# Kernel tuning notes

Measured on AMD Instinct MI355X. Metric: run time of the kernel, lower is better.

## Reference

```python
import jax, jax.numpy as jnp
import numpy as np

B, T, V, Dw, Df, H, L, F_ = 16, 96, 32000, 512, 512, 1024, 100, 64
EPS = 1e-8
SOS = 0


def setup_inputs() -> dict:
    key = jax.random.key(0)
    ks = jax.random.split(key, 24)
    rn = lambda k, s, sc=0.02: (jax.random.normal(k, s) * sc).astype(jnp.float32)
    pos_mask = (jax.random.uniform(ks[1], (B, F_, L)) < 0.3).astype(jnp.float32)
    pos_mask = jnp.maximum(pos_mask, jax.nn.one_hot(jnp.zeros((B, F_), jnp.int32), L))
    return {
        "fact_embeddings": rn(ks[0], (B, F_, Df), 1.0),
        "pos_mask": pos_mask,
        "emb": rn(ks[2], (V, Dw), 0.05),
        "W_ih": rn(ks[3], (4 * H, Df + Dw + L)),
        "W_hh": rn(ks[4], (4 * H, H)),
        "b_ih": jnp.zeros(4 * H, jnp.float32),
        "b_hh": jnp.zeros(4 * H, jnp.float32),
        "Wf1": rn(ks[5], (H, H + Df)), "bf1": jnp.zeros(H, jnp.float32),
        "Wf2": rn(ks[6], (Df, H)), "bf2": jnp.zeros(Df, jnp.float32),
        "Wc1": rn(ks[7], (H, H + Df)), "bc1": jnp.zeros(H, jnp.float32),
        "Wc2": rn(ks[8], (1, H)), "bc2": jnp.zeros(1, jnp.float32),
        "Wv1": rn(ks[9], (H, H + Df)), "bv1": jnp.zeros(H, jnp.float32),
        "Wv2": rn(ks[10], (Dw, H)), "bv2": jnp.zeros(Dw, jnp.float32),
        "Wp1": rn(ks[11], (H, H + Df)), "bp1": jnp.zeros(H, jnp.float32),
        "Wp2": rn(ks[12], (100, H)), "bp2": jnp.zeros(100, jnp.float32),
        "WP": rn(ks[13], (L, 100)), "bP": jnp.zeros(L, jnp.float32),
        "true_w": jax.random.randint(ks[14], (B, T), 0, L),
        "true_a": jax.random.randint(ks[15], (B, T), 0, F_),
        "true_z": jax.random.randint(ks[16], (B, T), 0, 2),
        "num_facts": jax.random.randint(ks[17], (B,), 1, F_),
    }


def reference(fact_embeddings, pos_mask, emb, W_ih, W_hh, b_ih, b_hh,
              Wf1, bf1, Wf2, bf2, Wc1, bc1, Wc2, bc2,
              Wv1, bv1, Wv2, bv2, Wp1, bp1, Wp2, bp2, WP, bP,
              true_w, true_a, true_z, num_facts):
    def mlp(x, W1, b1, W2, b2):
        return W2 @ jax.nn.relu(W1 @ x + b1) + b2

    def single(fe, pmask_b, tw, ta, tz, nf):
        # fe: [F_, Df]  pmask_b: [F_, L]  tw/ta/tz: [T]
        idx = jnp.arange(F_)
        valid = (idx < nf).astype(jnp.float32)
        attn_mask = jnp.where(idx == F_ - 1, 1.0, valid)  # NaF slot always allowed
        e_k = (fe * valid[:, None]).sum(0) / nf.astype(jnp.float32)

        def step(carry, inputs):
            a_prev, h, c, wv, wo = carry
            w_t, a_true, z_true = inputs
            x = jnp.concatenate([a_prev, wv, wo])  # [Df+Dw+L]
            gates = W_ih @ x + b_ih + W_hh @ h + b_hh
            i_g, f_g, g_g, o_g = jnp.split(gates, 4)
            c = jax.nn.sigmoid(f_g) * c + jax.nn.sigmoid(i_g) * jnp.tanh(g_g)
            h = jax.nn.sigmoid(o_g) * jnp.tanh(c)
            oe = jnp.concatenate([h, e_k])
            k_fact = mlp(oe, Wf1, bf1, Wf2, bf2)           # [Df]
            prob_a = jax.nn.softmax(fe @ k_fact)           # [F_]
            m = attn_mask * prob_a + EPS
            m = m / m.sum()
            log_m = jnp.log(m)
            a_idx = jnp.argmax(m)
            a_vec = fe[a_idx]
            oa = jnp.concatenate([h, a_vec])
            z = jax.nn.sigmoid(mlp(oa, Wc1, bc1, Wc2, bc2))[0]
            k_voca = mlp(oa, Wv1, bv1, Wv2, bv2)           # [Dw]
            log_w = jax.nn.log_softmax(emb @ k_voca)       # [V]
            k_pos = mlp(oa, Wp1, bp1, Wp2, bp2)            # [100]
            prob_pos = jax.nn.softmax(WP @ k_pos + bP)     # [L]
            mp = pmask_b[a_true] * prob_pos + EPS
            mp = mp / mp.sum()
            log_pos = jnp.log(mp)
            zf = z_true.astype(jnp.float32)
            loss = (-log_m[a_true]
                    + jnp.where(z_true == 0, -log_w[w_t], -log_pos[w_t])
                    - (zf * jnp.log(z) + (1.0 - zf) * jnp.log(1.0 - z)))
            wv_next = jnp.where(z_true == 0, emb[w_t], jnp.zeros(Dw, jnp.float32))
            wo_next = jnp.where(z_true == 0, jnp.zeros(L, jnp.float32), jax.nn.one_hot(w_t, L))
            return (a_vec, h, c, wv_next, wo_next), loss

        carry0 = (jnp.zeros(Df, jnp.float32), jnp.zeros(H, jnp.float32),
                  jnp.zeros(H, jnp.float32), emb[SOS], jnp.zeros(L, jnp.float32))
        _, losses = jax.lax.scan(step, carry0, (tw, ta, tz))
        return losses.sum()

    return jax.vmap(single)(fact_embeddings, pos_mask, true_w, true_a, true_z, num_facts).sum()
```

## Files before the change

### kernel.cpp

```cpp
#include <hip/hip_runtime.h>
#include <math.h>

#define TT 96
#define VV 32000
#define EPSF 1e-8f

typedef __attribute__((ext_vector_type(8))) short short8;
typedef __attribute__((ext_vector_type(4))) float f4v;

__device__ __forceinline__ float wsum64(float v){
  #pragma unroll
  for (int m=32;m>0;m>>=1) v += __shfl_xor(v,m);
  return v;
}
__device__ __forceinline__ float sigm(float x){ return 1.0f/(1.0f+expf(-x)); }
__device__ __forceinline__ float softplus(float x){ return x>20.0f ? x : log1pf(expf(x)); }
__device__ __forceinline__ float bf2f(unsigned short u){ return __uint_as_float(((unsigned)u)<<16); }
__device__ __forceinline__ unsigned short f2bf(float f){
  unsigned u = __float_as_uint(f);
  return (unsigned short)((u + 0x7fffu + ((u>>16)&1u)) >> 16);
}

__device__ __forceinline__ void st_dc(float* p, float v){
  __hip_atomic_store(p, v, __ATOMIC_RELAXED, __HIP_MEMORY_SCOPE_AGENT);
}
__device__ __forceinline__ void st_dc_i(int* p, int v){
  __hip_atomic_store(p, v, __ATOMIC_RELAXED, __HIP_MEMORY_SCOPE_AGENT);
}
__device__ __forceinline__ int ld_dc_i(const int* p){
  return __hip_atomic_load(p, __ATOMIC_RELAXED, __HIP_MEMORY_SCOPE_AGENT);
}
__device__ __forceinline__ float2 ld_dc_2(const float* p){
  union { unsigned long long u; float2 f; } cv;
  cv.u = __hip_atomic_load((const unsigned long long*)p, __ATOMIC_RELAXED, __HIP_MEMORY_SCOPE_AGENT);
  return cv.f;
}

__device__ __forceinline__ void gbar(unsigned* cnt, unsigned target){
  __syncthreads();
  if (threadIdx.x == 0){
    __hip_atomic_fetch_add(cnt, 1u, __ATOMIC_RELAXED, __HIP_MEMORY_SCOPE_AGENT);
    while (__hip_atomic_load(cnt, __ATOMIC_RELAXED, __HIP_MEMORY_SCOPE_AGENT) < target){
      __builtin_amdgcn_s_sleep(8);
    }
    asm volatile("" ::: "memory");
  }
  __syncthreads();
}

__device__ __forceinline__ void core_chunk(
  const float4* __restrict__ w0, const float4* __restrict__ w1,
  const float4* __restrict__ w2, const float4* __restrict__ w3,
  const float4* __restrict__ xl, int l, int g, float (&acc)[4][4])
{
  #pragma unroll
  for (int kt=0; kt<8; kt++){
    int i = kt*16 + l;
    float4 a0=w0[i], a1=w1[i], a2=w2[i], a3=w3[i];
    #pragma unroll
    for (int j=0;j<4;j++){
      float4 x = xl[(4*g+j)*129 + i];
      acc[0][j] += a0.x*x.x + a0.y*x.y + a0.z*x.z + a0.w*x.w;
      acc[1][j] += a1.x*x.x + a1.y*x.y + a1.z*x.z + a1.w*x.w;
      acc[2][j] += a2.x*x.x + a2.y*x.y + a2.z*x.z + a2.w*x.w;
      acc[3][j] += a3.x*x.x + a3.y*x.y + a3.z*x.z + a3.w*x.w;
    }
  }
}

__device__ __forceinline__ float reduce_pick(float (&acc)[4][4], int l){
  float r = 0.f;
  #pragma unroll
  for (int ri=0;ri<4;ri++)
  #pragma unroll
  for (int j=0;j<4;j++){
    float v = acc[ri][j];
    v += __shfl_xor(v,1); v += __shfl_xor(v,2);
    v += __shfl_xor(v,4); v += __shfl_xor(v,8);
    if (l == ri*4+j) r = v;
  }
  return r;
}

__global__ __launch_bounds__(256) void k_phase1(
  const float* __restrict__ Whh, float* __restrict__ hall,
  const float* __restrict__ Pw, const float* __restrict__ Pa,
  int* __restrict__ aall, float* __restrict__ c,
  const float* __restrict__ Wf1, const float* __restrict__ cf,
  float* __restrict__ tf,
  const float* __restrict__ Gb, const float* __restrict__ gb0,
  const int* __restrict__ ta, const int* __restrict__ nfp,
  float* __restrict__ loss, unsigned* __restrict__ bar)
{
  __shared__ float4 xl[16*129];
  __shared__ float sg[256];
  __shared__ float sS[64];
  int tid = threadIdx.x, lane = tid & 63, wave = tid >> 6;
  int l = lane & 15, g = lane >> 4;
  int wg = blockIdx.x;
  unsigned rnd = 0;

  for (int t=0; t<TT; t++){
    {
      int j0 = wg*4;
      const float4* h4 = (const float4*)hall + (size_t)t*4096;
      float acc[4][4] = {};
      for (int kc=0; kc<2; kc++){
        for (int idx=tid; idx<2048; idx+=256){
          int b = idx>>7, i = idx&127;
          xl[b*129+i] = h4[b*256 + kc*128 + i];
        }
        __syncthreads();
        const float4* w0 = (const float4*)(Whh + (size_t)(wave*1024 + j0+0)*1024) + kc*128;
        const float4* w1 = (const float4*)(Whh + (size_t)(wave*1024 + j0+1)*1024) + kc*128;
        const float4* w2 = (const float4*)(Whh + (size_t)(wave*1024 + j0+2)*1024) + kc*128;
        const float4* w3 = (const float4*)(Whh + (size_t)(wave*1024 + j0+3)*1024) + kc*128;
        core_chunk(w0,w1,w2,w3, xl, l, g, acc);
        __syncthreads();
      }
      float v = reduce_pick(acc, l);
      int r = l>>2;
      int b = g*4 + (l&3);
      int row = wave*1024 + j0 + r;
      float e = Pw[((size_t)(b*96+t))*4096 + row];
      if (t > 0){
        int ai = ld_dc_i(&aall[(t-1)*64 + b]);
        e += Pa[((size_t)(b*64+ai))*4096 + row];
      }
      sg[wave*64 + r*16 + b] = v + e;
      __syncthreads();
      if (tid < 64){
        int jj = j0 + (tid>>4), bb = tid&15;
        float ig = sg[  0 + (tid>>4)*16 + bb];
        float fg = sg[ 64 + (tid>>4)*16 + bb];
        float gg = sg[128 + (tid>>4)*16 + bb];
        float og = sg[192 + (tid>>4)*16 + bb];
        int ci = bb*1024 + jj;
        float cn = sigm(fg)*c[ci] + sigm(ig)*tanhf(gg);
        c[ci] = cn;
        st_dc(&hall[((size_t)(t+1)*16 + bb)*1024 + jj], sigm(og)*tanhf(cn));
      }
    }
    rnd++; gbar(bar, rnd*256u);

    if (wg < 64){
      int rl0 = wg*16 + wave*4;
      const float4* h4 = (const float4*)hall + (size_t)(t+1)*4096;
      float acc[4][4] = {};
      for (int kc=0; kc<2; kc++){
        for (int idx=tid; idx<2048; idx+=256){
          int b = idx>>7, i = idx&127;
          xl[b*129+i] = h4[b*256 + kc*128 + i];
        }
        __syncthreads();
        const float4* w0 = (const float4*)(Wf1 + (size_t)(rl0+0)*1536) + kc*128;
        const float4* w1 = (const float4*)(Wf1 + (size_t)(rl0+1)*1536) + kc*128;
        const float4* w2 = (const float4*)(Wf1 + (size_t)(rl0+2)*1536) + kc*128;
        const float4* w3 = (const float4*)(Wf1 + (size_t)(rl0+3)*1536) + kc*128;
        core_chunk(w0,w1,w2,w3, xl, l, g, acc);
        __syncthreads();
      }
      float v = reduce_pick(acc, l);
      int rl = rl0 + (l>>2);
      int b = g*4 + (l&3);
      st_dc(&tf[b*1024 + rl], fmaxf(v + cf[b*1024 + rl], 0.f));
    }
    rnd++; gbar(bar, rnd*256u);

    if (wg < 16){
      int b = wg;
      float* stf = (float*)xl;
      {
        const float* src = tf + b*1024;
        float2 c0 = ld_dc_2(src + 4*tid + 0);
        float2 c1 = ld_dc_2(src + 4*tid + 2);
        ((float2*)stf)[2*tid+0] = c0;
        ((float2*)stf)[2*tid+1] = c1;
      }
      __syncthreads();
      int f = tid>>2, q = tid&3;
      const float4* G4 = (const float4*)(Gb + (size_t)(b*64+f)*1024);
      const float4* st4 = (const float4*)stf;
      float acc = 0.f;
      for (int j=0;j<64;j++){
        int i = q*64 + j;
        float4 a = G4[i], x = st4[i];
        acc += a.x*x.x + a.y*x.y + a.z*x.z + a.w*x.w;
      }
      acc += __shfl_xor(acc,1);
      acc += __shfl_xor(acc,2);
      if (q==0) sS[f] = acc + gb0[b*64+f];
      __syncthreads();
      if (tid < 64){
        int nf = nfp[b];
        float s = sS[tid];
        float mx = s;
        #pragma unroll
        for (int m=32;m>0;m>>=1) mx = fmaxf(mx, __shfl_xor(mx,m));
        float p = expf(s - mx);
        float ps = wsum64(p);
        p /= ps;
        bool mask = (tid < nf) || (tid == 63);
        float mval = mask ? (p + EPSF) : EPSF;
        float msum = wsum64(mval);
        float bv = mval; int bi2 = tid;
        #pragma unroll
        for (int m=32;m>0;m>>=1){
          float ov = __shfl_xor(bv,m); int oi = __shfl_xor(bi2,m);
          if (ov > bv || (ov == bv && oi < bi2)){ bv = ov; bi2 = oi; }
        }
        int at = ta[b*TT + t];
        float mat = __shfl(mval, at);
        if (tid == 0){
          atomicAdd(loss, -(logf(mat) - logf(msum)));
          st_dc_i(&aall[t*64 + b], bi2);
        }
      }
      __syncthreads();
    }
    rnd++; gbar(bar, rnd*256u);
  }
}


__global__ __launch_bounds__(256) void k2_cvp(
  const float* __restrict__ Wc1, const float* __restrict__ Wv1,
  const float* __restrict__ Wp1, const float* __restrict__ hall,
  const float* __restrict__ Ph, const int* __restrict__ aall,
  const float* __restrict__ bc1, const float* __restrict__ bv1,
  const float* __restrict__ bp1, float* __restrict__ tcvp)
{
  __shared__ float4 xl[16*129];
  int tid = threadIdx.x, lane = tid & 63, wave = tid >> 6;
  int l = lane & 15, g = lane >> 4;
  int seg = blockIdx.x >> 6;
  int rl0 = (blockIdx.x & 63)*16 + wave*4;
  const float* W = (seg==0)?Wc1:(seg==1)?Wv1:Wp1;
  const float4* h4 = (const float4*)hall + (size_t)(16 + blockIdx.y*16)*256;
  float acc[4][4] = {};
  for (int kc=0; kc<2; kc++){
    for (int idx=tid; idx<2048; idx+=256){
      int cc = idx>>7, i = idx&127;
      xl[cc*129+i] = h4[cc*256 + kc*128 + i];
    }
    __syncthreads();
    const float4* w0 = (const float4*)(W + (size_t)(rl0+0)*1536) + kc*128;
    const float4* w1 = (const float4*)(W + (size_t)(rl0+1)*1536) + kc*128;
    const float4* w2 = (const float4*)(W + (size_t)(rl0+2)*1536) + kc*128;
    const float4* w3 = (const float4*)(W + (size_t)(rl0+3)*1536) + kc*128;
    core_chunk(w0,w1,w2,w3, xl, l, g, acc);
    __syncthreads();
  }
  float v = reduce_pick(acc, l);
  int rl = rl0 + (l>>2);
  int n = blockIdx.y*16 + g*4 + (l&3);
  int b = n & 15;
  int ai = aall[(n>>4)*64 + (n&15)];
  const float* bias = (seg==0)?bc1:(seg==1)?bv1:bp1;
  float vv = v + Ph[((size_t)(b*64+ai))*3072 + seg*1024 + rl] + bias[rl];
  tcvp[(size_t)n*3072 + seg*1024 + rl] = fmaxf(vv, 0.f);
}

__global__ __launch_bounds__(256) void k2_heads2(
  const float* __restrict__ Wv2, const float* __restrict__ bv2,
  const float* __restrict__ Wp2, const float* __restrict__ bp2,
  const float* __restrict__ Wc2, const float* __restrict__ bc2,
  const float* __restrict__ tcvp, unsigned short* __restrict__ kvh,
  float* __restrict__ kpall, float* __restrict__ zlall)
{
  __shared__ float4 xl[16*129];
  int tid = threadIdx.x, lane = tid & 63, wave = tid >> 6;
  int l = lane & 15, g = lane >> 4;
  int bx = blockIdx.x;
  int seg = (bx < 32) ? 0 : (bx < 39) ? 1 : 2;
  int rb  = (seg==0) ? bx*16 : (seg==1) ? (bx-32)*16 : 0;
  int rl0 = rb + wave*4;
  const float* WS = (seg==0)?Wv2:(seg==1)?Wp2:Wc2;
  int maxr = (seg==0)?511:(seg==1)?99:0;
  int xoff4 = (seg==0)?256:(seg==1)?512:0;
  const float4* X4 = (const float4*)tcvp;
  float acc[4][4] = {};
  for (int kc=0; kc<2; kc++){
    for (int idx=tid; idx<2048; idx+=256){
      int cc = idx>>7, i = idx&127;
      xl[cc*129+i] = X4[(size_t)(blockIdx.y*16+cc)*768 + xoff4 + kc*128 + i];
    }
    __syncthreads();
    const float4* w0 = (const float4*)(WS + (size_t)min(rl0+0,maxr)*1024) + kc*128;
    const float4* w1 = (const float4*)(WS + (size_t)min(rl0+1,maxr)*1024) + kc*128;
    const float4* w2 = (const float4*)(WS + (size_t)min(rl0+2,maxr)*1024) + kc*128;
    const float4* w3 = (const float4*)(WS + (size_t)min(rl0+3,maxr)*1024) + kc*128;
    core_chunk(w0,w1,w2,w3, xl, l, g, acc);
    __syncthreads();
  }
  float v = reduce_pick(acc, l);
  int rl = rl0 + (l>>2);
  int n = blockIdx.y*16 + g*4 + (l&3);
  if (seg==0) kvh[(size_t)n*512 + rl] = f2bf(v + bv2[rl]);
  else if (seg==1){ if (rl < 100) kpall[n*128 + rl] = v + bp2[rl]; }
  else { if (rl == 0) zlall[n] = v + bc2[0]; }
}

__global__ __launch_bounds__(256) void k2_vocab(
  const unsigned short* __restrict__ embh, const unsigned short* __restrict__ kvh,
  float2* __restrict__ part)
{
  int wid = blockIdx.x*4 + (threadIdx.x>>6);
  int lane = threadIdx.x & 63;
  int mtile = wid % 500, ntile = wid / 500;
  int mrow = mtile*64 + (lane&15);
  int ncol = ntile*64 + (lane&15);
  int ko = (lane>>4)*8;
  f4v acc[4][4];
  #pragma unroll
  for (int i=0;i<4;i++)
  #pragma unroll
  for (int j=0;j<4;j++)
  #pragma unroll
  for (int r=0;r<4;r++) acc[i][j][r] = 0.f;
  for (int kk=0; kk<512; kk+=32){
    short8 af[4], bfr[4];
    #pragma unroll
    for (int i=0;i<4;i++)
      af[i] = *(const short8*)(embh + (size_t)(mrow+16*i)*512 + kk + ko);
    #pragma unroll
    for (int i=0;i<4;i++)
      bfr[i] = *(const short8*)(kvh + (size_t)(ncol+16*i)*512 + kk + ko);
    #pragma unroll
    for (int i=0;i<4;i++)
      #pragma unroll
      for (int j=0;j<4;j++)
        acc[i][j] = __builtin_amdgcn_mfma_f32_16x16x32_bf16(af[i], bfr[j], acc[i][j], 0,0,0);
  }
  int q = lane>>4;
  #pragma unroll
  for (int j=0;j<4;j++){
    float mx = -3.4e38f;
    #pragma unroll
    for (int i=0;i<4;i++)
    #pragma unroll
    for (int r=0;r<4;r++) mx = fmaxf(mx, acc[i][j][r]);
    mx = fmaxf(mx, __shfl_xor(mx,16));
    mx = fmaxf(mx, __shfl_xor(mx,32));
    float s = 0.f;
    #pragma unroll
    for (int i=0;i<4;i++)
    #pragma unroll
    for (int r=0;r<4;r++) s += expf(acc[i][j][r] - mx);
    s += __shfl_xor(s,16);
    s += __shfl_xor(s,32);
    if (q==0){
      int col = ntile*64 + 16*j + (lane&15);
      part[(size_t)col*500 + mtile] = make_float2(mx, s);
    }
  }
}

__global__ __launch_bounds__(256) void k2_vfin(
  const float2* __restrict__ part, const unsigned short* __restrict__ embh,
  const unsigned short* __restrict__ kvh, const int* __restrict__ tw,
  const int* __restrict__ tz, float* __restrict__ loss)
{
  __shared__ float red[4];
  int n = blockIdx.x, tid = threadIdx.x;
  int t = n>>4, b = n&15;
  float mx = -3.4e38f;
  for (int i=tid; i<500; i+=256) mx = fmaxf(mx, part[(size_t)n*500+i].x);
  #pragma unroll
  for (int m=32;m>0;m>>=1) mx = fmaxf(mx, __shfl_xor(mx,m));
  if ((tid&63)==0) red[tid>>6] = mx;
  __syncthreads();
  float M = fmaxf(fmaxf(red[0],red[1]), fmaxf(red[2],red[3]));
  __syncthreads();
  float s = 0.f;
  for (int i=tid; i<500; i+=256){
    float2 p = part[(size_t)n*500+i];
    s += p.y * expf(p.x - M);
  }
  s = wsum64(s);
  if ((tid&63)==0) red[tid>>6] = s;
  __syncthreads();
  float S = red[0]+red[1]+red[2]+red[3];
  __syncthreads();
  int w = tw[b*96+t];
  float d = 0.f;
  {
    const unsigned short* er = embh + (size_t)w*512;
    const unsigned short* kr = kvh + (size_t)n*512;
    for (int i=tid; i<512; i+=256) d += bf2f(er[i])*bf2f(kr[i]);
  }
  d = wsum64(d);
  if ((tid&63)==0) red[tid>>6] = d;
  __syncthreads();
  if (tid==0 && tz[b*96+t]==0){
    float D = red[0]+red[1]+red[2]+red[3];
    atomicAdd(loss, -(D - (M + logf(S))));
  }
}

__global__ __launch_bounds__(128) void k2_posz(
  const float* __restrict__ kpall, const float* __restrict__ zlall,
  const float* __restrict__ WP, const float* __restrict__ bP,
  const float* __restrict__ pmask, const int* __restrict__ tw,
  const int* __restrict__ ta, const int* __restrict__ tz,
  float* __restrict__ loss)
{
  __shared__ float pp[100];
  int n = blockIdx.x, tid = threadIdx.x;
  int t = n>>4, b = n&15;
  if (tid < 100){
    float s = bP[tid];
    const float* wr = WP + tid*100;
    const float* kp = kpall + n*128;
    for (int j=0;j<100;j++) s += wr[j]*kp[j];
    pp[tid] = s;
  }
  __syncthreads();
  if (tid == 0){
    float u = zlall[n];
    int z = tz[b*96+t], w = tw[b*96+t], at = ta[b*96+t];
    float tot = z ? softplus(-u) : softplus(u);
    if (z){
      float mxv = -1e30f;
      for (int l2=0;l2<100;l2++) mxv = fmaxf(mxv, pp[l2]);
      float se = 0.f;
      for (int l2=0;l2<100;l2++) se += expf(pp[l2]-mxv);
      const float* pm = pmask + ((size_t)b*64 + at)*100;
      float msum = 0.f, mw = 0.f;
      for (int l2=0;l2<100;l2++){
        float m = pm[l2]*(expf(pp[l2]-mxv)/se) + EPSF;
        msum += m;
        if (l2==w) mw = m;
      }
      tot += -(logf(mw) - logf(msum));
    }
    atomicAdd(loss, tot);
  }
}


__global__ void k_cvt_emb(const float* __restrict__ emb, unsigned* __restrict__ out){
  const int n = VV*512/2;
  for (int idx = blockIdx.x*256 + threadIdx.x; idx < n; idx += gridDim.x*256){
    float2 v = ((const float2*)emb)[idx];
    unsigned a = __float_as_uint(v.x), b = __float_as_uint(v.y);
    unsigned ra = (a + 0x7fffu + ((a>>16)&1u)) >> 16;
    unsigned rb = (b + 0x7fffu + ((b>>16)&1u)) >> 16;
    out[idx] = ra | (rb<<16);
  }
}

__global__ void k_setup(const float* __restrict__ fe, const int* __restrict__ nfp,
                        float* __restrict__ e_k){
  int b = blockIdx.x, tid = threadIdx.x;
  int nf = nfp[b];
  for (int d=tid; d<512; d+=256){
    float s = 0.f;
    for (int f=0; f<nf; f++) s += fe[((size_t)b*64+f)*512 + d];
    e_k[b*512+d] = s/(float)nf;
  }
}

__global__ __launch_bounds__(256) void k_pre_pa(
  const float* __restrict__ Wih, const float* __restrict__ fe, float* __restrict__ Pa)
{
  __shared__ float4 xl[16*129];
  int tid = threadIdx.x, lane = tid & 63, wave = tid >> 6;
  int l = lane & 15, g = lane >> 4;
  int row0 = blockIdx.x*16 + wave*4;
  int c0 = blockIdx.y*16;
  const float4* fe4 = (const float4*)fe;
  for (int idx=tid; idx<2048; idx+=256){
    int cc = idx>>7, i = idx&127;
    xl[cc*129+i] = fe4[(size_t)(c0+cc)*128 + i];
  }
  __syncthreads();
  const float4* w0 = (const float4*)(Wih + (size_t)(row0+0)*1124);
  const float4* w1 = (const float4*)(Wih + (size_t)(row0+1)*1124);
  const float4* w2 = (const float4*)(Wih + (size_t)(row0+2)*1124);
  const float4* w3 = (const float4*)(Wih + (size_t)(row0+3)*1124);
  float acc[4][4] = {};
  core_chunk(w0,w1,w2,w3, xl, l, g, acc);
  float v = reduce_pick(acc, l);
  int row = row0 + (l>>2), c = c0 + g*4 + (l&3);
  Pa[(size_t)c*4096 + row] = v;
}

__global__ __launch_bounds__(256) void k_pre_ph(
  const float* __restrict__ Wc1, const float* __restrict__ Wv1,
  const float* __restrict__ Wp1, const float* __restrict__ fe, float* __restrict__ Ph)
{
  __shared__ float4 xl[16*129];
  int tid = threadIdx.x, lane = tid & 63, wave = tid >> 6;
  int l = lane & 15, g = lane >> 4;
  int row0 = blockIdx.x*16 + wave*4;
  int head = row0 >> 10, rl0 = row0 & 1023;
  const float* W = (head==0)?Wc1:(head==1)?Wv1:Wp1;
  int c0 = blockIdx.y*16;
  const float4* fe4 = (const float4*)fe;
  for (int idx=tid; idx<2048; idx+=256){
    int cc = idx>>7, i = idx&127;
    xl[cc*129+i] = fe4[(size_t)(c0+cc)*128 + i];
  }
  __syncthreads();
  const float4* w0 = (const float4*)(W + (size_t)(rl0+0)*1536 + 1024);
  const float4* w1 = (const float4*)(W + (size_t)(rl0+1)*1536 + 1024);
  const float4* w2 = (const float4*)(W + (size_t)(rl0+2)*1536 + 1024);
  const float4* w3 = (const float4*)(W + (size_t)(rl0+3)*1536 + 1024);
  float acc[4][4] = {};
  core_chunk(w0,w1,w2,w3, xl, l, g, acc);
  float v = reduce_pick(acc, l);
  int row = row0 + (l>>2), c = c0 + g*4 + (l&3);
  Ph[(size_t)c*3072 + row] = v;
}

__global__ __launch_bounds__(256) void k_pre_pw(
  const float* __restrict__ Wih, const float* __restrict__ emb,
  const int* __restrict__ tw, const int* __restrict__ tz,
  const float* __restrict__ bih, const float* __restrict__ bhh,
  float* __restrict__ Pw)
{
  __shared__ float4 xl[16*129];
  int tid = threadIdx.x, lane = tid & 63, wave = tid >> 6;
  int l = lane & 15, g = lane >> 4;
  int row0 = blockIdx.x*16 + wave*4;
  int c0 = blockIdx.y*16;
  for (int idx=tid; idx<2048; idx+=256){
    int cc = idx>>7, i = idx&127;
    int c = c0+cc, b = c/96, t2 = c - b*96;
    int w=0, z=0;
    if (t2>0){ w = tw[b*96+t2-1]; z = tz[b*96+t2-1]; }
    float4 v = make_float4(0.f,0.f,0.f,0.f);
    if (z==0) v = ((const float4*)emb)[(size_t)w*128 + i];
    xl[cc*129+i] = v;
  }
  __syncthreads();
  const float4* w0 = (const float4*)(Wih + (size_t)(row0+0)*1124 + 512);
  const float4* w1 = (const float4*)(Wih + (size_t)(row0+1)*1124 + 512);
  const float4* w2 = (const float4*)(Wih + (size_t)(row0+2)*1124 + 512);
  const float4* w3 = (const float4*)(Wih + (size_t)(row0+3)*1124 + 512);
  float acc[4][4] = {};
  core_chunk(w0,w1,w2,w3, xl, l, g, acc);
  float v = reduce_pick(acc, l);
  int row = row0 + (l>>2), c = c0 + g*4 + (l&3);
  int b = c/96, t2 = c - b*96;
  int w=0, z=0;
  if (t2>0){ w = tw[b*96+t2-1]; z = tz[b*96+t2-1]; }
  v += bih[row] + bhh[row];
  if (z) v += Wih[(size_t)row*1124 + 1024 + w];
  Pw[(size_t)c*4096 + row] = v;
}

__global__ __launch_bounds__(256) void k_pre_cf(
  const float* __restrict__ Wf1, const float* __restrict__ bf1,
  const float* __restrict__ e_k, float* __restrict__ cf)
{
  __shared__ float4 xl[16*129];
  int tid = threadIdx.x, lane = tid & 63, wave = tid >> 6;
  int l = lane & 15, g = lane >> 4;
  int row0 = blockIdx.x*16 + wave*4;
  const float4* ek4 = (const float4*)e_k;
  for (int idx=tid; idx<2048; idx+=256){
    int cc = idx>>7, i = idx&127;
    xl[cc*129+i] = ek4[cc*128 + i];
  }
  __syncthreads();
  const float4* w0 = (const float4*)(Wf1 + (size_t)(row0+0)*1536 + 1024);
  const float4* w1 = (const float4*)(Wf1 + (size_t)(row0+1)*1536 + 1024);
  const float4* w2 = (const float4*)(Wf1 + (size_t)(row0+2)*1536 + 1024);
  const float4* w3 = (const float4*)(Wf1 + (size_t)(row0+3)*1536 + 1024);
  float acc[4][4] = {};
  core_chunk(w0,w1,w2,w3, xl, l, g, acc);
  float v = reduce_pick(acc, l);
  int row = row0 + (l>>2), b = g*4 + (l&3);
  cf[b*1024 + row] = v + bf1[row];
}

__global__ __launch_bounds__(256) void k_pre_g(
  const float* __restrict__ Wf2, const float* __restrict__ fe, float* __restrict__ Gb)
{
  __shared__ float fs[16][128];
  int tid = threadIdx.x;
  int r0 = blockIdx.x*16;
  int k0 = blockIdx.y*256;
  float acc[16] = {};
  for (int dc=0; dc<4; dc++){
    for (int idx=tid; idx<2048; idx+=256){
      int r = idx>>7, d = idx&127;
      fs[r][d] = fe[(size_t)(r0+r)*512 + dc*128 + d];
    }
    __syncthreads();
    for (int d=0; d<128; d++){
      float w = Wf2[(size_t)(dc*128+d)*1024 + k0 + tid];
      #pragma unroll
      for (int r=0;r<16;r++) acc[r] += fs[r][d]*w;
    }
    __syncthreads();
  }
  #pragma unroll
  for (int r=0;r<16;r++) Gb[(size_t)(r0+r)*1024 + k0 + tid] = acc[r];
}

__global__ __launch_bounds__(256) void k_gb0(
  const float* __restrict__ fe, const float* __restrict__ bf2, float* __restrict__ gb0)
{
  int b = blockIdx.x;
  int f = threadIdx.x>>2, q = threadIdx.x&3;
  const float4* fe4 = (const float4*)(fe + ((size_t)b*64+f)*512);
  const float4* b4 = (const float4*)bf2;
  float acc = 0.f;
  for (int j=0;j<32;j++){
    int i = q*32+j;
    float4 a = fe4[i], x = b4[i];
    acc += a.x*x.x + a.y*x.y + a.z*x.z + a.w*x.w;
  }
  acc += __shfl_xor(acc,1);
  acc += __shfl_xor(acc,2);
  if (q==0) gb0[b*64+f] = acc;
}

__global__ void k_out(const float* __restrict__ loss, float* __restrict__ out){
  out[0] = loss[0];
}

extern "C" void kernel_launch(void* const* d_in, const int* in_sizes, int n_in,
                              void* d_out, int out_size, void* d_ws, size_t ws_size,
                              hipStream_t stream)
{
  const float* fe   = (const float*)d_in[0];
  const float* pmask= (const float*)d_in[1];
  const float* emb  = (const float*)d_in[2];
  const float* Wih  = (const float*)d_in[3];
  const float* Whh  = (const float*)d_in[4];
  const float* bih  = (const float*)d_in[5];
  const float* bhh  = (const float*)d_in[6];
  const float* Wf1  = (const float*)d_in[7];
  const float* bf1  = (const float*)d_in[8];
  const float* Wf2  = (const float*)d_in[9];
  const float* bf2  = (const float*)d_in[10];
  const float* Wc1  = (const float*)d_in[11];
  const float* bc1  = (const float*)d_in[12];
  const float* Wc2  = (const float*)d_in[13];
  const float* bc2  = (const float*)d_in[14];
  const float* Wv1  = (const float*)d_in[15];
  const float* bv1  = (const float*)d_in[16];
  const float* Wv2  = (const float*)d_in[17];
  const float* bv2  = (const float*)d_in[18];
  const float* Wp1  = (const float*)d_in[19];
  const float* bp1  = (const float*)d_in[20];
  const float* Wp2  = (const float*)d_in[21];
  const float* bp2  = (const float*)d_in[22];
  const float* WP   = (const float*)d_in[23];
  const float* bP   = (const float*)d_in[24];
  const int* tw  = (const int*)d_in[25];
  const int* ta  = (const int*)d_in[26];
  const int* tz  = (const int*)d_in[27];
  const int* nfp = (const int*)d_in[28];

  float* w = (float*)d_ws;
  float*    loss  = w + 0;
  unsigned* bar   = (unsigned*)(w + 8);
  float*    c     = w + 64;
  float*    hall  = w + 16448;
  int*      aall  = (int*)(w + 1605696);
  float*    tf    = w + 1611840;
  float*    gb0   = w + 1628224;
  float*    e_k   = w + 1629248;
  float*    cf    = w + 1637440;
  float*    kpall = w + 1653824;
  float*    zlall = w + 1850432;
  float*    tcvp  = w + 1851968;
  float*    Gb    = w + 1851968;
  float2*   part  = (float2*)(w + 6570560);
  unsigned short* kvh = (unsigned short*)(w + 8106560);
  float*    Pa    = w + 8499776;
  float*    Ph    = w + 12694080;
  float*    Pw    = w + 15839808;
  unsigned* embbf = (unsigned*)(w + 22131264);
  const unsigned short* embh = (const unsigned short*)embbf;

  hipMemsetAsync(d_ws, 0, (size_t)32832*4, stream);
  k_cvt_emb<<<8192,256,0,stream>>>(emb, embbf);
  k_setup<<<16,256,0,stream>>>(fe, nfp, e_k);
  k_pre_pa<<<dim3(256,64),256,0,stream>>>(Wih, fe, Pa);
  k_pre_ph<<<dim3(192,64),256,0,stream>>>(Wc1, Wv1, Wp1, fe, Ph);
  k_pre_pw<<<dim3(256,96),256,0,stream>>>(Wih, emb, tw, tz, bih, bhh, Pw);
  k_pre_cf<<<64,256,0,stream>>>(Wf1, bf1, e_k, cf);
  k_pre_g<<<dim3(64,4),256,0,stream>>>(Wf2, fe, Gb);
  k_gb0<<<16,256,0,stream>>>(fe, bf2, gb0);

  k_phase1<<<256,256,0,stream>>>(Whh, hall, Pw, Pa, aall, c, Wf1, cf, tf,
                                 Gb, gb0, ta, nfp, loss, bar);

  k2_cvp<<<dim3(192,96),256,0,stream>>>(Wc1, Wv1, Wp1, hall, Ph, aall,
                                        bc1, bv1, bp1, tcvp);
  k2_heads2<<<dim3(40,96),256,0,stream>>>(Wv2, bv2, Wp2, bp2, Wc2, bc2,
                                          tcvp, kvh, kpall, zlall);
  k2_vocab<<<3000,256,0,stream>>>(embh, kvh, part);
  k2_vfin<<<1536,256,0,stream>>>(part, embh, kvh, tw, tz, loss);
  k2_posz<<<1536,128,0,stream>>>(kpall, zlall, WP, bP, pmask, tw, ta, tz, loss);
  k_out<<<1,1,0,stream>>>(loss, (float*)d_out);
}
```

Measured before the change: 5.404 ms.

## Replace grid barriers with sharded counters and point-to-point flag waits

The persistent recurrence kernel used three global barriers per timestep. Now the first barrier spreads its arrivals over eight padded counters, and block 0 alone polls them and publishes a release epoch. The other two barriers become targeted waits: the attention blocks wait on a sharded counter from the 64 Wf1 blocks, and the LSTM blocks spin on the argmax flags, stored as index+1 so zero means not ready. tf is double-buffered to make this safe, and the Pw/Pa loads become nontemporal. This shortens the serial per-step sync chain but adds spin-polling and memory-ordering risk, since only relaxed atomics are used.

After: 4.630 ms. 14.3% less time.

```diff
diff --git a/kernel.cpp b/kernel.cpp
--- a/kernel.cpp
+++ b/kernel.cpp
@@ -30,20 +30,34 @@
 __device__ __forceinline__ int ld_dc_i(const int* p){
   return __hip_atomic_load(p, __ATOMIC_RELAXED, __HIP_MEMORY_SCOPE_AGENT);
 }
+__device__ __forceinline__ unsigned ld_cnt(const unsigned* p){
+  return __hip_atomic_load(p, __ATOMIC_RELAXED, __HIP_MEMORY_SCOPE_AGENT);
+}
 __device__ __forceinline__ float2 ld_dc_2(const float* p){
   union { unsigned long long u; float2 f; } cv;
   cv.u = __hip_atomic_load((const unsigned long long*)p, __ATOMIC_RELAXED, __HIP_MEMORY_SCOPE_AGENT);
   return cv.f;
 }
 
-__device__ __forceinline__ void gbar(unsigned* cnt, unsigned target){
-  __syncthreads();
-  if (threadIdx.x == 0){
-    __hip_atomic_fetch_add(cnt, 1u, __ATOMIC_RELAXED, __HIP_MEMORY_SCOPE_AGENT);
-    while (__hip_atomic_load(cnt, __ATOMIC_RELAXED, __HIP_MEMORY_SCOPE_AGENT) < target){
-      __builtin_amdgcn_s_sleep(8);
-    }
-    asm volatile("" ::: "memory");
+__device__ __forceinline__ void bar_full(unsigned* cntA, unsigned* rel, unsigned epoch){
+  __syncthreads();
+  if (threadIdx.x == 0)
+    __hip_atomic_fetch_add(cntA + (blockIdx.x & 7)*64, 1u, __ATOMIC_RELAXED, __HIP_MEMORY_SCOPE_AGENT);
+  if (blockIdx.x == 0){
+    if (threadIdx.x < 64){
+      unsigned tgt = epoch * 32u;
+      while (true){
+        unsigned v = (threadIdx.x < 8) ? ld_cnt(cntA + threadIdx.x*64) : tgt;
+        if (__all(v >= tgt)) break;
+        __builtin_amdgcn_s_sleep(1);
+      }
+      if (threadIdx.x == 0)
+        __hip_atomic_store(rel, epoch, __ATOMIC_RELAXED, __HIP_MEMORY_SCOPE_AGENT);
+    }
+  } else {
+    if (threadIdx.x == 0){
+      while (ld_cnt(rel) < epoch) __builtin_amdgcn_s_sleep(1);
+    }
   }
   __syncthreads();
 }
@@ -90,15 +104,17 @@
   float* __restrict__ tf,
   const float* __restrict__ Gb, const float* __restrict__ gb0,
   const int* __restrict__ ta, const int* __restrict__ nfp,
-  float* __restrict__ loss, unsigned* __restrict__ bar)
+  float* __restrict__ loss,
+  unsigned* __restrict__ cntA, unsigned* __restrict__ cntB,
+  unsigned* __restrict__ rel)
 {
   __shared__ float4 xl[16*129];
   __shared__ float sg[256];
   __shared__ float sS[64];
+  __shared__ int   sai[16];
   int tid = threadIdx.x, lane = tid & 63, wave = tid >> 6;
   int l = lane & 15, g = lane >> 4;
   int wg = blockIdx.x;
-  unsigned rnd = 0;
 
   for (int t=0; t<TT; t++){
     {
@@ -119,13 +135,22 @@
         __syncthreads();
       }
       float v = reduce_pick(acc, l);
+      if (t > 0 && tid < 64){
+        bool need = (tid < 16);
+        while (true){
+          int vv = need ? ld_dc_i(&aall[(t-1)*64 + tid]) : 1;
+          if (__all(vv != 0)){ if (need) sai[tid] = vv - 1; break; }
+          __builtin_amdgcn_s_sleep(1);
+        }
+      }
+      __syncthreads();
       int r = l>>2;
       int b = g*4 + (l&3);
       int row = wave*1024 + j0 + r;
-      float e = Pw[((size_t)(b*96+t))*4096 + row];
+      float e = __builtin_nontemporal_load(Pw + ((size_t)(b*96+t))*4096 + row);
       if (t > 0){
-        int ai = ld_dc_i(&aall[(t-1)*64 + b]);
-        e += Pa[((size_t)(b*64+ai))*4096 + row];
+        int ai = sai[b];
+        e += __builtin_nontemporal_load(Pa + ((size_t)(b*64+ai))*4096 + row);
       }
       sg[wave*64 + r*16 + b] = v + e;
       __syncthreads();
@@ -141,7 +166,7 @@
         st_dc(&hall[((size_t)(t+1)*16 + bb)*1024 + jj], sigm(og)*tanhf(cn));
       }
     }
-    rnd++; gbar(bar, rnd*256u);
+    bar_full(cntA, rel, (unsigned)(t+1));
 
     if (wg < 64){
       int rl0 = wg*16 + wave*4;
@@ -163,15 +188,28 @@
       float v = reduce_pick(acc, l);
       int rl = rl0 + (l>>2);
       int b = g*4 + (l&3);
-      st_dc(&tf[b*1024 + rl], fmaxf(v + cf[b*1024 + rl], 0.f));
-    }
-    rnd++; gbar(bar, rnd*256u);
-
-    if (wg < 16){
-      int b = wg;
+      float* tfb = tf + (t&1)*16384;
+      st_dc(&tfb[b*1024 + rl], fmaxf(v + cf[b*1024 + rl], 0.f));
+      __syncthreads();
+      if (tid == 0)
+        __hip_atomic_fetch_add(cntB + (wg&7)*64, 1u, __ATOMIC_RELAXED, __HIP_MEMORY_SCOPE_AGENT);
+    }
+
+    if (wg >= 240){
+      int b = wg - 240;
+      if (tid < 64){
+        unsigned tgt = (unsigned)(t+1) * 8u;
+        while (true){
+          unsigned vv = (tid < 8) ? ld_cnt(cntB + tid*64) : tgt;
+          if (__all(vv >= tgt)) break;
+          __builtin_amdgcn_s_sleep(1);
+        }
+      }
+      __syncthreads();
+      const float* tfb = tf + (t&1)*16384;
       float* stf = (float*)xl;
       {
-        const float* src = tf + b*1024;
+        const float* src = tfb + b*1024;
         float2 c0 = ld_dc_2(src + 4*tid + 0);
         float2 c1 = ld_dc_2(src + 4*tid + 2);
         ((float2*)stf)[2*tid+0] = c0;
@@ -213,12 +251,11 @@
         float mat = __shfl(mval, at);
         if (tid == 0){
           atomicAdd(loss, -(logf(mat) - logf(msum)));
-          st_dc_i(&aall[t*64 + b], bi2);
+          st_dc_i(&aall[t*64 + b], bi2 + 1);
         }
       }
       __syncthreads();
     }
-    rnd++; gbar(bar, rnd*256u);
   }
 }
 
@@ -255,7 +292,7 @@
   int rl = rl0 + (l>>2);
   int n = blockIdx.y*16 + g*4 + (l&3);
   int b = n & 15;
-  int ai = aall[(n>>4)*64 + (n&15)];
+  int ai = aall[(n>>4)*64 + (n&15)] - 1;
   const float* bias = (seg==0)?bc1:(seg==1)?bv1:bp1;
   float vv = v + Ph[((size_t)(b*64+ai))*3072 + seg*1024 + rl] + bias[rl];
   tcvp[(size_t)n*3072 + seg*1024 + rl] = fmaxf(vv, 0.f);
@@ -659,27 +696,30 @@
 
   float* w = (float*)d_ws;
   float*    loss  = w + 0;
-  unsigned* bar   = (unsigned*)(w + 8);
-  float*    c     = w + 64;
-  float*    hall  = w + 16448;
-  int*      aall  = (int*)(w + 1605696);
-  float*    tf    = w + 1611840;
-  float*    gb0   = w + 1628224;
-  float*    e_k   = w + 1629248;
-  float*    cf    = w + 1637440;
-  float*    kpall = w + 1653824;
-  float*    zlall = w + 1850432;
-  float*    tcvp  = w + 1851968;
-  float*    Gb    = w + 1851968;
-  float2*   part  = (float2*)(w + 6570560);
-  unsigned short* kvh = (unsigned short*)(w + 8106560);
-  float*    Pa    = w + 8499776;
-  float*    Ph    = w + 12694080;
-  float*    Pw    = w + 15839808;
-  unsigned* embbf = (unsigned*)(w + 22131264);
+  unsigned* cntA  = (unsigned*)(w + 64);
+  unsigned* cntB  = (unsigned*)(w + 576);
+  unsigned* rel   = (unsigned*)(w + 1088);
+  float*    c     = w + 2048;
+  float*    hall  = w + 18432;
+  int*      aall  = (int*)(w + 1607680);
+  float*    tf    = w + 1613824;
+  float*    gb0   = w + 1646592;
+  float*    e_k   = w + 1647616;
+  float*    cf    = w + 1655808;
+  float*    kpall = w + 1672192;
+  float*    zlall = w + 1868800;
+  float*    tcvp  = w + 1870336;
+  float*    Gb    = w + 1870336;
+  float2*   part  = (float2*)(w + 6588928);
+  unsigned short* kvh = (unsigned short*)(w + 8124928);
+  float*    Pa    = w + 8518144;
+  float*    Ph    = w + 12712448;
+  float*    Pw    = w + 15858176;
+  unsigned* embbf = (unsigned*)(w + 22149632);
   const unsigned short* embh = (const unsigned short*)embbf;
 
-  hipMemsetAsync(d_ws, 0, (size_t)32832*4, stream);
+  hipMemsetAsync(d_ws, 0, (size_t)34816*4, stream);
+  hipMemsetAsync((void*)aall, 0, (size_t)96*64*4, stream);
   k_cvt_emb<<<8192,256,0,stream>>>(emb, embbf);
   k_setup<<<16,256,0,stream>>>(fe, nfp, e_k);
   k_pre_pa<<<dim3(256,64),256,0,stream>>>(Wih, fe, Pa);
@@ -690,7 +730,7 @@
   k_gb0<<<16,256,0,stream>>>(fe, bf2, gb0);
 
   k_phase1<<<256,256,0,stream>>>(Whh, hall, Pw, Pa, aall, c, Wf1, cf, tf,
-                                 Gb, gb0, ta, nfp, loss, bar);
+                                 Gb, gb0, ta, nfp, loss, cntA, cntB, rel);
 
   k2_cvp<<<dim3(192,96),256,0,stream>>>(Wc1, Wv1, Wp1, hall, Ph, aall,
                                         bc1, bv1, bp1, tcvp);
```
